# Kernel tuning notes

Hardware: AMD Instinct MI355X
Metric: run time of the kernel (lower is better)

Reference implementation:

```python
import jax, jax.numpy as jnp
import numpy as np

N_NODES = 100000
N_EDGES = 1600000
FEAT = 512
CLS = 64
HID = 200  # each hop layer output width; 3 hops -> 600 concat


def spmm(row, col, vals, x):
    # out[r] = sum_{e: row[e]==r} vals[e] * x[col[e]]  -- sparse A @ x
    return jax.ops.segment_sum(x[col] * vals[:, None], row, num_segments=x.shape[0])


def setup_inputs() -> dict:
    key = jax.random.key(0)
    ks = jax.random.split(key, 12)
    adj_index = jax.random.randint(ks[0], (2, N_EDGES), 0, N_NODES, dtype=jnp.int64)
    # scale like a normalized adjacency (~1/avg_degree) to keep powers stable
    adj_values = jax.random.uniform(ks[1], (N_EDGES,), dtype=jnp.float32) * (1.0 / 16.0)
    features = jax.random.normal(ks[2], (N_NODES, FEAT), dtype=jnp.float32)
    s1 = (2.0 / (FEAT + HID)) ** 0.5
    s2 = (2.0 / (3 * HID + HID)) ** 0.5
    sf = (2.0 / (3 * HID + CLS)) ** 0.5
    W1 = jax.random.normal(ks[3], (3, FEAT, HID), dtype=jnp.float32) * s1
    b1 = jax.random.normal(ks[4], (3, HID), dtype=jnp.float32) * 0.01
    W2 = jax.random.normal(ks[5], (3, 3 * HID, HID), dtype=jnp.float32) * s2
    b2 = jax.random.normal(ks[6], (3, HID), dtype=jnp.float32) * 0.01
    Wfc = jax.random.normal(ks[7], (3 * HID, CLS), dtype=jnp.float32) * sf
    bfc = jax.random.normal(ks[8], (CLS,), dtype=jnp.float32) * 0.01
    return {"adj_index": adj_index, "adj_values": adj_values, "features": features,
            "W1": W1, "b1": b1, "W2": W2, "b2": b2, "Wfc": Wfc, "bfc": bfc}


def reference(adj_index, adj_values, features, W1, b1, W2, b2, Wfc, bfc):
    # Inference mode: dropout is identity.
    row, col = adj_index[0], adj_index[1]
    # upper (sparse) layers: linear + bias + relu, then (iterations-1) spmm hops
    outs1 = []
    for i in range(3):  # iterations = i + 1
        h = jax.nn.relu(features @ W1[i] + b1[i][None, :])
        for _ in range(i):
            h = spmm(row, col, adj_values, h)
        outs1.append(h)
    abstract1 = jnp.concatenate(outs1, axis=1)  # [N, 600]
    # bottom (dense) layers: linear, (iterations-1) spmm hops, then + bias
    outs2 = []
    for i in range(3):
        h = abstract1 @ W2[i]
        for _ in range(i):
            h = spmm(row, col, adj_values, h)
        h = h + b2[i][None, :]
        outs2.append(h)
    abstract2 = jnp.concatenate(outs2, axis=1)  # [N, 600]
    node_emb = abstract2 @ Wfc + bfc  # [N, CLS]
    predictions = jax.nn.log_softmax(node_emb, axis=1)
    return node_emb, predictions
```

## Files before the change

kernel.cpp:

```cpp
#include <hip/hip_runtime.h>

typedef unsigned short u16;
typedef unsigned int u32;
typedef __attribute__((ext_vector_type(8))) short short8;
typedef __attribute__((ext_vector_type(4))) float f32x4;
typedef __attribute__((ext_vector_type(4))) u32 u32x4;
typedef __attribute__((ext_vector_type(2))) u32 u32x2;

#define NN 100000
#define PAD 640

__device__ __forceinline__ float b2f(u16 u) {
    union { u32 i; float f; } v; v.i = ((u32)u) << 16; return v.f;
}
__device__ __forceinline__ u16 f2b(float f) {
    union { float f; u32 i; } v; v.f = f;
    u32 x = v.i;
    return (u16)((x + 0x7FFFu + ((x >> 16) & 1u)) >> 16);
}
__device__ __forceinline__ u32 pack2(float lo, float hi) {
    return (u32)f2b(lo) | ((u32)f2b(hi) << 16);
}
__device__ __forceinline__ float rdf(const void* p, size_t i, int f) {
    return f ? ((const float*)p)[i] : b2f(((const u16*)p)[i]);
}
__device__ __forceinline__ void gload16(const u16* g, u16* l) {
    __builtin_amdgcn_global_load_lds(
        (const __attribute__((address_space(1))) void*)g,
        (__attribute__((address_space(3))) void*)l, 16, 0, 0);
}

__global__ void probe_k(const int* __restrict__ idx,
                        const void* avals, const void* feats, const void* W1,
                        const void* b1, const void* W2, const void* b2,
                        const void* Wfc, const void* bfc,
                        int* __restrict__ flags) {
    if (threadIdx.x != 0 || blockIdx.x != 0) return;
    int z = 1;
    for (int i = 0; i < 128; ++i)
        if (idx[2 * i + 1] != 0) { z = 0; break; }
    flags[0] = z;
    const void* ts[8] = {avals, feats, W1, b1, W2, b2, Wfc, bfc};
    const int ns[8] = {256, 256, 256, 128, 256, 128, 256, 32};
    for (int t = 0; t < 8; ++t) {
        const u16* p = (const u16*)ts[t];
        int n = ns[t], bad = 0;
        for (int i = 0; i < n; ++i) {
            int e = (p[2 * i] >> 7) & 0xFF;
            if (e >= 133) bad++;
        }
        flags[1 + t] = (bad * 8 >= n) ? 1 : 0;
    }
}

__device__ __forceinline__ int load_row(const int* idx, int E, int f, int e) {
    return f ? idx[2 * e] : idx[e];
}
__device__ __forceinline__ int load_col(const int* idx, int E, int f, int e) {
    return f ? idx[2 * E + 2 * e] : idx[E + e];
}

__global__ void featconv_k(const void* __restrict__ src, u16* __restrict__ dst,
                           const int* __restrict__ flags) {
    int i = blockIdx.x * 256 + threadIdx.x;
    if (i >= NN * 512) return;
    int f = flags[2];
    dst[i] = f ? f2b(((const float*)src)[i]) : ((const u16*)src)[i];
}
__global__ void w1t_k(const void* __restrict__ W1, u16* __restrict__ w1t,
                      const int* __restrict__ flags) {
    int i = blockIdx.x * 256 + threadIdx.x;
    if (i >= 640 * 512) return;
    int n = i >> 9, k = i & 511;
    float v = 0.f;
    if (n < 600) {
        int ib = n / 200, c = n % 200;
        v = rdf(W1, (size_t)ib * 102400 + (size_t)k * 200 + c, flags[3]);
    }
    w1t[i] = f2b(v);
}
__global__ void w2t_k(const void* __restrict__ W2, u16* __restrict__ w2t,
                      const int* __restrict__ flags) {
    int i = blockIdx.x * 256 + threadIdx.x;
    if (i >= 640 * 640) return;
    int n = i / 640, k = i % 640;
    float v = 0.f;
    if (n < 600 && k < 600) {
        int ib = n / 200, c = n % 200;
        v = rdf(W2, (size_t)ib * 120000 + (size_t)k * 200 + c, flags[5]);
    }
    w2t[i] = f2b(v);
}
__global__ void wfct_k(const void* __restrict__ Wfc, u16* __restrict__ wfct,
                       const int* __restrict__ flags) {
    int i = blockIdx.x * 256 + threadIdx.x;
    if (i >= 64 * 640) return;
    int n = i / 640, k = i % 640;
    float v = 0.f;
    if (k < 600) v = rdf(Wfc, (size_t)k * 64 + n, flags[7]);
    wfct[i] = f2b(v);
}
__global__ void bconv_k(const void* __restrict__ b1, const void* __restrict__ b2,
                        const void* __restrict__ bfc, float* __restrict__ o,
                        const int* __restrict__ flags) {
    int i = blockIdx.x * 256 + threadIdx.x;
    if (i < 600) o[i] = rdf(b1, i, flags[4]);
    else if (i < 1200) o[i] = rdf(b2, i - 600, flags[6]);
    else if (i < 1264) o[i] = rdf(bfc, i - 1200, flags[8]);
}

__global__ void count_k(const int* __restrict__ idx, int E, const int* __restrict__ flags,
                        int* __restrict__ counts) {
    int e = blockIdx.x * 256 + threadIdx.x;
    if (e >= E) return;
    int r = load_row(idx, E, flags[0], e);
    if ((u32)r >= NN) return;
    atomicAdd(&counts[r], 1);
}

__global__ void chunksum_k(const int* __restrict__ counts, int* __restrict__ chsum) {
    __shared__ int sm[256];
    int c = blockIdx.x, t = threadIdx.x;
    int base = c * 1024, s = 0;
    for (int i = t; i < 1024; i += 256) {
        int g = base + i;
        if (g < NN) s += counts[g];
    }
    sm[t] = s; __syncthreads();
    for (int off = 128; off; off >>= 1) {
        if (t < off) sm[t] += sm[t + off];
        __syncthreads();
    }
    if (t == 0) chsum[c] = sm[0];
}

__global__ void chscan_k(const int* __restrict__ chsum, int nch, int* __restrict__ choff,
                         int* __restrict__ row_ptr, int E) {
    if (threadIdx.x == 0 && blockIdx.x == 0) {
        int run = 0;
        for (int c = 0; c < nch; ++c) { choff[c] = run; run += chsum[c]; }
        row_ptr[NN] = run;
    }
}

__global__ __launch_bounds__(1024) void scan_k(const int* __restrict__ counts,
                                               const int* __restrict__ choff,
                                               int* __restrict__ row_ptr,
                                               int* __restrict__ cursor) {
    __shared__ int sm[1024];
    int c = blockIdx.x, t = threadIdx.x;
    int g = c * 1024 + t;
    int v = (g < NN) ? counts[g] : 0;
    sm[t] = v;
    __syncthreads();
    for (int off = 1; off < 1024; off <<= 1) {
        int add = (t >= off) ? sm[t - off] : 0;
        __syncthreads();
        sm[t] += add;
        __syncthreads();
    }
    if (g < NN) {
        int ex = choff[c] + sm[t] - v;
        row_ptr[g] = ex;
        cursor[g] = ex;
    }
}

__global__ void scatter_k(const int* __restrict__ idx, const void* __restrict__ avals, int E,
                          const int* __restrict__ flags, int* __restrict__ cursor,
                          int* __restrict__ colsS, float* __restrict__ valsS) {
    int e = blockIdx.x * 256 + threadIdx.x;
    if (e >= E) return;
    int f = flags[0];
    int r = load_row(idx, E, f, e);
    if ((u32)r >= NN) return;
    int c = load_col(idx, E, f, e);
    if ((u32)c >= NN) c = 0;
    int p = atomicAdd(&cursor[r], 1);
    colsS[p] = c;
    valsS[p] = rdf(avals, e, flags[1]);
}

__global__ __launch_bounds__(256) void gemm128_k(
    const u16* __restrict__ A, const u16* __restrict__ Bt,
    u16* __restrict__ C, float* __restrict__ Cf,
    const float* __restrict__ bias, int bias_n, int relu,
    int M, int K, int lda, int ldc) {
    __shared__ u16 As[128 * 32];
    __shared__ u16 Bs[128 * 32];
    const int tid = threadIdx.x;
    const int wave = tid >> 6, lane = tid & 63;
    const int bm = blockIdx.x * 128, bn = blockIdx.y * 128;
    const int wrow = (wave >> 1) * 64, wcol = (wave & 1) * 64;
    const int l15 = lane & 15, l4 = lane >> 4;
    f32x4 acc[4][4] = {};

    const int c0 = wave * 2;
    const int rowA0 = c0 * 16 + (lane >> 2);
    const int rowA1 = rowA0 + 16;
    const int colE = (lane & 3) * 8;
    int gr0 = bm + rowA0; if (gr0 >= M) gr0 = M - 1;
    int gr1 = bm + rowA1; if (gr1 >= M) gr1 = M - 1;
    const u16* a0p = A + (size_t)gr0 * lda + colE;
    const u16* a1p = A + (size_t)gr1 * lda + colE;
    const u16* b0p = Bt + (size_t)(bn + rowA0) * K + colE;
    const u16* b1p = Bt + (size_t)(bn + rowA1) * K + colE;
    u16* lA0 = As + c0 * 512;
    u16* lA1 = As + c0 * 512 + 512;
    u16* lB0 = Bs + c0 * 512;
    u16* lB1 = Bs + c0 * 512 + 512;

    for (int k0 = 0; k0 < K; k0 += 32) {
        __syncthreads();
        gload16(a0p + k0, lA0);
        gload16(a1p + k0, lA1);
        gload16(b0p + k0, lB0);
        gload16(b1p + k0, lB1);
        __syncthreads();
        short8 af[4], bf[4];
#pragma unroll
        for (int t = 0; t < 4; ++t) {
            af[t] = *(const short8*)&As[(wrow + t * 16 + l15) * 32 + l4 * 8];
            bf[t] = *(const short8*)&Bs[(wcol + t * 16 + l15) * 32 + l4 * 8];
        }
#pragma unroll
        for (int mi = 0; mi < 4; ++mi)
#pragma unroll
            for (int ni = 0; ni < 4; ++ni)
                acc[mi][ni] = __builtin_amdgcn_mfma_f32_16x16x32_bf16(
                    af[mi], bf[ni], acc[mi][ni], 0, 0, 0);
    }

#pragma unroll
    for (int mi = 0; mi < 4; ++mi)
#pragma unroll
        for (int ni = 0; ni < 4; ++ni)
#pragma unroll
            for (int r4 = 0; r4 < 4; ++r4) {
                int row = bm + wrow + mi * 16 + l4 * 4 + r4;
                int col = bn + wcol + ni * 16 + l15;
                if (row < M) {
                    float v = acc[mi][ni][r4];
                    if (bias && col < bias_n) v += bias[col];
                    if (relu) v = fmaxf(v, 0.0f);
                    if (C) C[(size_t)row * ldc + col] = f2b(v);
                    if (Cf) Cf[(size_t)row * ldc + col] = v;
                }
            }
}

__global__ __launch_bounds__(256) void gemm_k(
    const u16* __restrict__ A, const u16* __restrict__ Bt,
    u16* __restrict__ C, float* __restrict__ Cf,
    const float* __restrict__ bias, int bias_n, int relu,
    int M, int K, int lda, int ldc) {
    __shared__ u16 As[64][40];
    __shared__ u16 Bs[64][40];
    const int tid = threadIdx.x;
    const int wave = tid >> 6, lane = tid & 63;
    const int bm = blockIdx.x * 64, bn = blockIdx.y * 64;
    const int wr = (wave >> 1) * 32, wc = (wave & 1) * 32;
    const int l15 = lane & 15, l4 = lane >> 4;
    f32x4 acc[2][2] = {};

    const int srow = tid >> 2;
    const int skoff = (tid & 3) * 8;
    const bool arow_ok = (bm + srow) < M;
    const u16* aptr = A + (size_t)(bm + srow) * lda + skoff;
    const u16* bptr = Bt + (size_t)(bn + srow) * K + skoff;

    for (int k0 = 0; k0 < K; k0 += 32) {
        short8 av = {};
        if (arow_ok) av = *(const short8*)(aptr + k0);
        short8 bv = *(const short8*)(bptr + k0);
        __syncthreads();
        *(short8*)&As[srow][skoff] = av;
        *(short8*)&Bs[srow][skoff] = bv;
        __syncthreads();
        short8 a0 = *(const short8*)&As[wr + l15][l4 * 8];
        short8 a1 = *(const short8*)&As[wr + 16 + l15][l4 * 8];
        short8 bb0 = *(const short8*)&Bs[wc + l15][l4 * 8];
        short8 bb1 = *(const short8*)&Bs[wc + 16 + l15][l4 * 8];
        acc[0][0] = __builtin_amdgcn_mfma_f32_16x16x32_bf16(a0, bb0, acc[0][0], 0, 0, 0);
        acc[0][1] = __builtin_amdgcn_mfma_f32_16x16x32_bf16(a0, bb1, acc[0][1], 0, 0, 0);
        acc[1][0] = __builtin_amdgcn_mfma_f32_16x16x32_bf16(a1, bb0, acc[1][0], 0, 0, 0);
        acc[1][1] = __builtin_amdgcn_mfma_f32_16x16x32_bf16(a1, bb1, acc[1][1], 0, 0, 0);
    }

#pragma unroll
    for (int mi = 0; mi < 2; ++mi)
#pragma unroll
        for (int ni = 0; ni < 2; ++ni)
#pragma unroll
            for (int r = 0; r < 4; ++r) {
                int row = bm + wr + mi * 16 + l4 * 4 + r;
                int col = bn + wc + ni * 16 + l15;
                if (row < M) {
                    float v = acc[mi][ni][r];
                    if (bias && col < bias_n) v += bias[col];
                    if (relu) v = fmaxf(v, 0.0f);
                    if (C) C[(size_t)row * ldc + col] = f2b(v);
                    if (Cf) Cf[(size_t)row * ldc + col] = v;
                }
            }
}

__global__ __launch_bounds__(256) void spmm400_k(
    const int* __restrict__ row_ptr, const int* __restrict__ cols,
    const float* __restrict__ vals, int E,
    const u16* __restrict__ X, u16* __restrict__ Y1, u16* __restrict__ Yt,
    const float* __restrict__ bias1) {
    int r = blockIdx.x * 4 + (threadIdx.x >> 6);
    if (r >= NN) return;
    int lane = threadIdx.x & 63;
    int s = row_ptr[r], e = row_ptr[r + 1];
    if (e > E) e = E;
    if (s < 0) s = 0;
    if (s > e) s = e;
    float a[8] = {0.f, 0.f, 0.f, 0.f, 0.f, 0.f, 0.f, 0.f};
    const bool act = lane < 50;
    const u32* xb = (const u32*)X;
    int i = s;
    for (; i + 2 <= e; i += 2) {
        int ca = cols[i]; if ((u32)ca >= NN) ca = 0;
        int cb = cols[i + 1]; if ((u32)cb >= NN) cb = 0;
        float va = vals[i], vb = vals[i + 1];
        if (act) {
            u32x4 ga = *(const u32x4*)(xb + (size_t)ca * 320 + lane * 4);
            u32x4 gb = *(const u32x4*)(xb + (size_t)cb * 320 + lane * 4);
#pragma unroll
            for (int q = 0; q < 4; ++q) {
                union { u32 i; float f; } lo, hi;
                lo.i = ga[q] << 16; hi.i = ga[q] & 0xffff0000u;
                a[2 * q] = fmaf(va, lo.f, a[2 * q]);
                a[2 * q + 1] = fmaf(va, hi.f, a[2 * q + 1]);
                lo.i = gb[q] << 16; hi.i = gb[q] & 0xffff0000u;
                a[2 * q] = fmaf(vb, lo.f, a[2 * q]);
                a[2 * q + 1] = fmaf(vb, hi.f, a[2 * q + 1]);
            }
        }
    }
    if (i < e) {
        int ca = cols[i]; if ((u32)ca >= NN) ca = 0;
        float va = vals[i];
        if (act) {
            u32x4 ga = *(const u32x4*)(xb + (size_t)ca * 320 + lane * 4);
#pragma unroll
            for (int q = 0; q < 4; ++q) {
                union { u32 i; float f; } lo, hi;
                lo.i = ga[q] << 16; hi.i = ga[q] & 0xffff0000u;
                a[2 * q] = fmaf(va, lo.f, a[2 * q]);
                a[2 * q + 1] = fmaf(va, hi.f, a[2 * q + 1]);
            }
        }
    }
    if (bias1 && lane < 25) {
#pragma unroll
        for (int q = 0; q < 8; ++q) a[q] += bias1[lane * 8 + q];
    }
    u32x4 o;
    o[0] = pack2(a[0], a[1]); o[1] = pack2(a[2], a[3]);
    o[2] = pack2(a[4], a[5]); o[3] = pack2(a[6], a[7]);
    if (lane < 25) {
        *(u32x4*)((u32*)Y1 + (size_t)r * 320 + lane * 4) = o;
    } else if (lane < 50) {
        *(u32x4*)((u32*)Yt + (size_t)r * 100 + (lane - 25) * 4) = o;
    }
}

__global__ __launch_bounds__(256) void spmm200_k(
    const int* __restrict__ row_ptr, const int* __restrict__ cols,
    const float* __restrict__ vals, int E,
    const u16* __restrict__ X, int ldx,
    u16* __restrict__ Y, int ldy,
    const float* __restrict__ bias) {
    int r = blockIdx.x * 4 + (threadIdx.x >> 6);
    if (r >= NN) return;
    int lane = threadIdx.x & 63;
    int s = row_ptr[r], e = row_ptr[r + 1];
    if (e > E) e = E;
    if (s < 0) s = 0;
    if (s > e) s = e;
    float a[4] = {0.f, 0.f, 0.f, 0.f};
    const bool act = lane < 50;
    const int ldxw = ldx >> 1, ldyw = ldy >> 1;
    const u32* xb = (const u32*)X;
    int i = s;
    for (; i + 2 <= e; i += 2) {
        int ca = cols[i]; if ((u32)ca >= NN) ca = 0;
        int cb = cols[i + 1]; if ((u32)cb >= NN) cb = 0;
        float va = vals[i], vb = vals[i + 1];
        if (act) {
            u32x2 ga = *(const u32x2*)(xb + (size_t)ca * ldxw + lane * 2);
            u32x2 gb = *(const u32x2*)(xb + (size_t)cb * ldxw + lane * 2);
#pragma unroll
            for (int q = 0; q < 2; ++q) {
                union { u32 i; float f; } lo, hi;
                lo.i = ga[q] << 16; hi.i = ga[q] & 0xffff0000u;
                a[2 * q] = fmaf(va, lo.f, a[2 * q]);
                a[2 * q + 1] = fmaf(va, hi.f, a[2 * q + 1]);
                lo.i = gb[q] << 16; hi.i = gb[q] & 0xffff0000u;
                a[2 * q] = fmaf(vb, lo.f, a[2 * q]);
                a[2 * q + 1] = fmaf(vb, hi.f, a[2 * q + 1]);
            }
        }
    }
    if (i < e) {
        int ca = cols[i]; if ((u32)ca >= NN) ca = 0;
        float va = vals[i];
        if (act) {
            u32x2 ga = *(const u32x2*)(xb + (size_t)ca * ldxw + lane * 2);
#pragma unroll
            for (int q = 0; q < 2; ++q) {
                union { u32 i; float f; } lo, hi;
                lo.i = ga[q] << 16; hi.i = ga[q] & 0xffff0000u;
                a[2 * q] = fmaf(va, lo.f, a[2 * q]);
                a[2 * q + 1] = fmaf(va, hi.f, a[2 * q + 1]);
            }
        }
    }
    if (bias && act) {
#pragma unroll
        for (int q = 0; q < 4; ++q) a[q] += bias[lane * 4 + q];
    }
    if (act) {
        u32x2 o;
        o[0] = pack2(a[0], a[1]); o[1] = pack2(a[2], a[3]);
        *(u32x2*)((u32*)Y + (size_t)r * ldyw + lane * 2) = o;
    }
}

__global__ void copyblk_k(const u16* __restrict__ src, u16* __restrict__ dst) {
    int i = blockIdx.x * 256 + threadIdx.x;
    if (i >= NN * 100) return;
    int r = i / 100, c = i % 100;
    ((u32*)dst)[(size_t)r * 320 + c] = ((const u32*)src)[(size_t)r * 320 + c];
}
__global__ void zeropad_k(u16* __restrict__ dst) {
    int i = blockIdx.x * 256 + threadIdx.x;
    if (i >= NN * 20) return;
    int r = i / 20, c = i % 20;
    ((u32*)dst)[(size_t)r * 320 + 300 + c] = 0u;
}
__global__ void copybias_k(const u16* __restrict__ src, u16* __restrict__ dst,
                           const float* __restrict__ bias) {
    int i = blockIdx.x * 256 + threadIdx.x;
    if (i >= NN * 200) return;
    int r = i / 200, c = i % 200;
    dst[(size_t)r * 640 + c] = f2b(b2f(src[(size_t)r * 640 + c]) + bias[c]);
}

__global__ void softmax_k(const float* __restrict__ ne, float* __restrict__ out) {
    int r = blockIdx.x * 4 + (threadIdx.x >> 6);
    if (r >= NN) return;
    int lane = threadIdx.x & 63;
    float v = ne[(size_t)r * 64 + lane];
    float m = v;
    for (int off = 32; off; off >>= 1) m = fmaxf(m, __shfl_xor(m, off, 64));
    float e = expf(v - m);
    float ssum = e;
    for (int off = 32; off; off >>= 1) ssum += __shfl_xor(ssum, off, 64);
    out[(size_t)r * 64 + lane] = v - m - logf(ssum);
}

extern "C" void kernel_launch(void* const* d_in, const int* in_sizes, int n_in,
                              void* d_out, int out_size, void* d_ws, size_t ws_size,
                              hipStream_t stream) {
    const int* adj_idx = (const int*)d_in[0];
    const void* adj_vals = d_in[1];
    const void* feats = d_in[2];
    const void* W1 = d_in[3];
    const void* b1 = d_in[4];
    const void* W2 = d_in[5];
    const void* b2 = d_in[6];
    const void* Wfc = d_in[7];
    const void* bfc = d_in[8];
    const int E = in_sizes[1];
    (void)n_in; (void)out_size; (void)ws_size;

    char* ws = (char*)d_ws;
    size_t off = 0;
    auto alloc = [&](size_t b) { size_t o = off; off += (b + 255) & ~(size_t)255; return o; };
    u16* buf0 = (u16*)(ws + alloc((size_t)NN * PAD * 2));
    u16* buf1 = (u16*)(ws + alloc((size_t)NN * PAD * 2));
    u16* hop = (u16*)(ws + alloc((size_t)NN * 200 * 2));
    u16* w1t = (u16*)(ws + alloc((size_t)640 * 512 * 2));
    u16* w2t = (u16*)(ws + alloc((size_t)640 * 640 * 2));
    u16* wfct = (u16*)(ws + alloc((size_t)64 * 640 * 2));
    float* biasf = (float*)(ws + alloc(1264 * 4));
    int* counts = (int*)(ws + alloc((size_t)NN * 4));
    int* cursor = (int*)(ws + alloc((size_t)NN * 4));
    int* row_ptr = (int*)(ws + alloc((size_t)(NN + 1) * 4));
    int* chsum = (int*)(ws + alloc(4096));
    int* choff = (int*)(ws + alloc(4096));
    int* flags = (int*)(ws + alloc(256));
    int* colsS = (int*)(ws + alloc((size_t)E * 4));
    float* valsS = (float*)(ws + alloc((size_t)E * 4));

    u16* featsB = buf1;
    float* out_ne = (float*)d_out;
    float* out_pred = out_ne + (size_t)NN * 64;

    probe_k<<<1, 64, 0, stream>>>(adj_idx, adj_vals, feats, W1, b1, W2, b2, Wfc, bfc, flags);
    featconv_k<<<(NN * 512 + 255) / 256, 256, 0, stream>>>(feats, featsB, flags);
    w1t_k<<<(640 * 512 + 255) / 256, 256, 0, stream>>>(W1, w1t, flags);
    w2t_k<<<(640 * 640 + 255) / 256, 256, 0, stream>>>(W2, w2t, flags);
    wfct_k<<<(64 * 640 + 255) / 256, 256, 0, stream>>>(Wfc, wfct, flags);
    bconv_k<<<5, 256, 0, stream>>>(b1, b2, bfc, biasf, flags);

    hipMemsetAsync(counts, 0, NN * 4, stream);
    count_k<<<(E + 255) / 256, 256, 0, stream>>>(adj_idx, E, flags, counts);
    const int NCH = (NN + 1023) / 1024;
    chunksum_k<<<NCH, 256, 0, stream>>>(counts, chsum);
    chscan_k<<<1, 64, 0, stream>>>(chsum, NCH, choff, row_ptr, E);
    scan_k<<<NCH, 1024, 0, stream>>>(counts, choff, row_ptr, cursor);
    scatter_k<<<(E + 255) / 256, 256, 0, stream>>>(adj_idx, adj_vals, E, flags, cursor, colsS, valsS);

    dim3 g128((NN + 127) / 128, PAD / 128);
    gemm128_k<<<g128, 256, 0, stream>>>(featsB, w1t, buf0, nullptr, biasf, 600, 1, NN, 512, 512, PAD);
    copyblk_k<<<(NN * 100 + 255) / 256, 256, 0, stream>>>(buf0, buf1);
    zeropad_k<<<(NN * 20 + 255) / 256, 256, 0, stream>>>(buf1);
    spmm400_k<<<(NN + 3) / 4, 256, 0, stream>>>(row_ptr, colsS, valsS, E,
                                                buf0 + 200, buf1 + 200, hop, nullptr);
    spmm200_k<<<(NN + 3) / 4, 256, 0, stream>>>(row_ptr, colsS, valsS, E,
                                                hop, 200, buf1 + 400, PAD, nullptr);
    gemm128_k<<<g128, 256, 0, stream>>>(buf1, w2t, buf0, nullptr, nullptr, 0, 0, NN, PAD, PAD, PAD);
    copybias_k<<<(NN * 200 + 255) / 256, 256, 0, stream>>>(buf0, buf1, biasf + 600);
    spmm400_k<<<(NN + 3) / 4, 256, 0, stream>>>(row_ptr, colsS, valsS, E,
                                                buf0 + 200, buf1 + 200, hop, biasf + 800);
    spmm200_k<<<(NN + 3) / 4, 256, 0, stream>>>(row_ptr, colsS, valsS, E,
                                                hop, 200, buf1 + 400, PAD, biasf + 1000);
    dim3 gC((NN + 63) / 64, 1);
    gemm_k<<<gC, 256, 0, stream>>>(buf1, wfct, nullptr, out_ne, biasf + 1200, 64, 0, NN, PAD, PAD, 64);
    softmax_k<<<(NN + 3) / 4, 256, 0, stream>>>(out_ne, out_pred);
}
```

Before: 1.727 ms.

## Interleave CSR col/val pairs, unroll SpMM by four, merge prep kernels, swap GEMM grid

Stores each sorted edge's column and value together as one 8-byte pair, so the SpMM kernels fetch both with a single load instead of two separate arrays. The SpMM inner loops are unrolled from two to four edges to put more independent gathers in flight. The three weight-transpose kernels and the bias conversion are merged into one launch. The GEMM grid is transposed so blocks sharing an A row-tile run next to each other, which may improve L2 reuse of A.

```diff
diff --git a/kernel.cpp b/kernel.cpp
--- a/kernel.cpp
+++ b/kernel.cpp
@@ -21,6 +21,9 @@
 __device__ __forceinline__ u32 pack2(float lo, float hi) {
     return (u32)f2b(lo) | ((u32)f2b(hi) << 16);
 }
+__device__ __forceinline__ float u2f(u32 u) {
+    union { u32 i; float f; } v; v.i = u; return v.f;
+}
 __device__ __forceinline__ float rdf(const void* p, size_t i, int f) {
     return f ? ((const float*)p)[i] : b2f(((const u16*)p)[i]);
 }
@@ -28,6 +31,20 @@
     __builtin_amdgcn_global_load_lds(
         (const __attribute__((address_space(1))) void*)g,
         (__attribute__((address_space(3))) void*)l, 16, 0, 0);
+}
+__device__ __forceinline__ void acc8(float* a, u32x4 g, float v) {
+#pragma unroll
+    for (int q = 0; q < 4; ++q) {
+        a[2 * q] = fmaf(v, u2f(g[q] << 16), a[2 * q]);
+        a[2 * q + 1] = fmaf(v, u2f(g[q] & 0xffff0000u), a[2 * q + 1]);
+    }
+}
+__device__ __forceinline__ void acc4(float* a, u32x2 g, float v) {
+#pragma unroll
+    for (int q = 0; q < 2; ++q) {
+        a[2 * q] = fmaf(v, u2f(g[q] << 16), a[2 * q]);
+        a[2 * q + 1] = fmaf(v, u2f(g[q] & 0xffff0000u), a[2 * q + 1]);
+    }
 }
 
 __global__ void probe_k(const int* __restrict__ idx,
@@ -67,46 +84,43 @@
     int f = flags[2];
     dst[i] = f ? f2b(((const float*)src)[i]) : ((const u16*)src)[i];
 }
-__global__ void w1t_k(const void* __restrict__ W1, u16* __restrict__ w1t,
-                      const int* __restrict__ flags) {
-    int i = blockIdx.x * 256 + threadIdx.x;
-    if (i >= 640 * 512) return;
-    int n = i >> 9, k = i & 511;
-    float v = 0.f;
-    if (n < 600) {
-        int ib = n / 200, c = n % 200;
-        v = rdf(W1, (size_t)ib * 102400 + (size_t)k * 200 + c, flags[3]);
-    }
-    w1t[i] = f2b(v);
-}
-__global__ void w2t_k(const void* __restrict__ W2, u16* __restrict__ w2t,
-                      const int* __restrict__ flags) {
-    int i = blockIdx.x * 256 + threadIdx.x;
-    if (i >= 640 * 640) return;
-    int n = i / 640, k = i % 640;
-    float v = 0.f;
-    if (n < 600 && k < 600) {
-        int ib = n / 200, c = n % 200;
-        v = rdf(W2, (size_t)ib * 120000 + (size_t)k * 200 + c, flags[5]);
-    }
-    w2t[i] = f2b(v);
-}
-__global__ void wfct_k(const void* __restrict__ Wfc, u16* __restrict__ wfct,
+__global__ void prep_k(const void* __restrict__ W1, const void* __restrict__ W2,
+                       const void* __restrict__ Wfc,
+                       const void* __restrict__ b1, const void* __restrict__ b2,
+                       const void* __restrict__ bfc,
+                       u16* __restrict__ w1t, u16* __restrict__ w2t,
+                       u16* __restrict__ wfct, float* __restrict__ biasf,
                        const int* __restrict__ flags) {
     int i = blockIdx.x * 256 + threadIdx.x;
-    if (i >= 64 * 640) return;
-    int n = i / 640, k = i % 640;
-    float v = 0.f;
-    if (k < 600) v = rdf(Wfc, (size_t)k * 64 + n, flags[7]);
-    wfct[i] = f2b(v);
-}
-__global__ void bconv_k(const void* __restrict__ b1, const void* __restrict__ b2,
-                        const void* __restrict__ bfc, float* __restrict__ o,
-                        const int* __restrict__ flags) {
-    int i = blockIdx.x * 256 + threadIdx.x;
-    if (i < 600) o[i] = rdf(b1, i, flags[4]);
-    else if (i < 1200) o[i] = rdf(b2, i - 600, flags[6]);
-    else if (i < 1264) o[i] = rdf(bfc, i - 1200, flags[8]);
+    if (i < 327680) {
+        int n = i >> 9, k = i & 511;
+        float v = 0.f;
+        if (n < 600) {
+            int ib = n / 200, c = n % 200;
+            v = rdf(W1, (size_t)ib * 102400 + (size_t)k * 200 + c, flags[3]);
+        }
+        w1t[i] = f2b(v);
+    } else if (i < 737280) {
+        int j = i - 327680;
+        int n = j / 640, k = j % 640;
+        float v = 0.f;
+        if (n < 600 && k < 600) {
+            int ib = n / 200, c = n % 200;
+            v = rdf(W2, (size_t)ib * 120000 + (size_t)k * 200 + c, flags[5]);
+        }
+        w2t[j] = f2b(v);
+    } else if (i < 778240) {
+        int j = i - 737280;
+        int n = j / 640, k = j % 640;
+        float v = 0.f;
+        if (k < 600) v = rdf(Wfc, (size_t)k * 64 + n, flags[7]);
+        wfct[j] = f2b(v);
+    } else if (i < 779504) {
+        int j = i - 778240;
+        if (j < 600) biasf[j] = rdf(b1, j, flags[4]);
+        else if (j < 1200) biasf[j] = rdf(b2, j - 600, flags[6]);
+        else biasf[j] = rdf(bfc, j - 1200, flags[8]);
+    }
 }
 
 __global__ void count_k(const int* __restrict__ idx, int E, const int* __restrict__ flags,
@@ -168,7 +182,7 @@
 
 __global__ void scatter_k(const int* __restrict__ idx, const void* __restrict__ avals, int E,
                           const int* __restrict__ flags, int* __restrict__ cursor,
-                          int* __restrict__ colsS, float* __restrict__ valsS) {
+                          u32x2* __restrict__ cvS) {
     int e = blockIdx.x * 256 + threadIdx.x;
     if (e >= E) return;
     int f = flags[0];
@@ -177,8 +191,10 @@
     int c = load_col(idx, E, f, e);
     if ((u32)c >= NN) c = 0;
     int p = atomicAdd(&cursor[r], 1);
-    colsS[p] = c;
-    valsS[p] = rdf(avals, e, flags[1]);
+    float v = rdf(avals, e, flags[1]);
+    union { float f; u32 i; } vb; vb.f = v;
+    u32x2 o; o[0] = (u32)c; o[1] = vb.i;
+    cvS[p] = o;
 }
 
 __global__ __launch_bounds__(256) void gemm128_k(
@@ -190,7 +206,7 @@
     __shared__ u16 Bs[128 * 32];
     const int tid = threadIdx.x;
     const int wave = tid >> 6, lane = tid & 63;
-    const int bm = blockIdx.x * 128, bn = blockIdx.y * 128;
+    const int bm = blockIdx.y * 128, bn = blockIdx.x * 128;
     const int wrow = (wave >> 1) * 64, wcol = (wave & 1) * 64;
     const int l15 = lane & 15, l4 = lane >> 4;
     f32x4 acc[4][4] = {};
@@ -306,8 +322,7 @@
 }
 
 __global__ __launch_bounds__(256) void spmm400_k(
-    const int* __restrict__ row_ptr, const int* __restrict__ cols,
-    const float* __restrict__ vals, int E,
+    const int* __restrict__ row_ptr, const u32x2* __restrict__ cv, int E,
     const u16* __restrict__ X, u16* __restrict__ Y1, u16* __restrict__ Yt,
     const float* __restrict__ bias1) {
     int r = blockIdx.x * 4 + (threadIdx.x >> 6);
@@ -320,38 +335,31 @@
     float a[8] = {0.f, 0.f, 0.f, 0.f, 0.f, 0.f, 0.f, 0.f};
     const bool act = lane < 50;
     const u32* xb = (const u32*)X;
+    const size_t lo = (size_t)lane * 4;
     int i = s;
-    for (; i + 2 <= e; i += 2) {
-        int ca = cols[i]; if ((u32)ca >= NN) ca = 0;
-        int cb = cols[i + 1]; if ((u32)cb >= NN) cb = 0;
-        float va = vals[i], vb = vals[i + 1];
+    for (; i + 4 <= e; i += 4) {
+        u32x2 p0 = cv[i], p1 = cv[i + 1], p2 = cv[i + 2], p3 = cv[i + 3];
+        int c0 = p0[0]; if ((u32)c0 >= NN) c0 = 0;
+        int c1 = p1[0]; if ((u32)c1 >= NN) c1 = 0;
+        int c2 = p2[0]; if ((u32)c2 >= NN) c2 = 0;
+        int c3 = p3[0]; if ((u32)c3 >= NN) c3 = 0;
         if (act) {
-            u32x4 ga = *(const u32x4*)(xb + (size_t)ca * 320 + lane * 4);
-            u32x4 gb = *(const u32x4*)(xb + (size_t)cb * 320 + lane * 4);
-#pragma unroll
-            for (int q = 0; q < 4; ++q) {
-                union { u32 i; float f; } lo, hi;
-                lo.i = ga[q] << 16; hi.i = ga[q] & 0xffff0000u;
-                a[2 * q] = fmaf(va, lo.f, a[2 * q]);
-                a[2 * q + 1] = fmaf(va, hi.f, a[2 * q + 1]);
-                lo.i = gb[q] << 16; hi.i = gb[q] & 0xffff0000u;
-                a[2 * q] = fmaf(vb, lo.f, a[2 * q]);
-                a[2 * q + 1] = fmaf(vb, hi.f, a[2 * q + 1]);
-            }
-        }
-    }
-    if (i < e) {
-        int ca = cols[i]; if ((u32)ca >= NN) ca = 0;
-        float va = vals[i];
+            u32x4 g0 = *(const u32x4*)(xb + (size_t)c0 * 320 + lo);
+            u32x4 g1 = *(const u32x4*)(xb + (size_t)c1 * 320 + lo);
+            u32x4 g2 = *(const u32x4*)(xb + (size_t)c2 * 320 + lo);
+            u32x4 g3 = *(const u32x4*)(xb + (size_t)c3 * 320 + lo);
+            acc8(a, g0, u2f(p0[1]));
+            acc8(a, g1, u2f(p1[1]));
+            acc8(a, g2, u2f(p2[1]));
+            acc8(a, g3, u2f(p3[1]));
+        }
+    }
+    for (; i < e; ++i) {
+        u32x2 p = cv[i];
+        int c = p[0]; if ((u32)c >= NN) c = 0;
         if (act) {
-            u32x4 ga = *(const u32x4*)(xb + (size_t)ca * 320 + lane * 4);
-#pragma unroll
-            for (int q = 0; q < 4; ++q) {
-                union { u32 i; float f; } lo, hi;
-                lo.i = ga[q] << 16; hi.i = ga[q] & 0xffff0000u;
-                a[2 * q] = fmaf(va, lo.f, a[2 * q]);
-                a[2 * q + 1] = fmaf(va, hi.f, a[2 * q + 1]);
-            }
+            u32x4 g = *(const u32x4*)(xb + (size_t)c * 320 + lo);
+            acc8(a, g, u2f(p[1]));
         }
     }
     if (bias1 && lane < 25) {
@@ -369,8 +377,7 @@
 }
 
 __global__ __launch_bounds__(256) void spmm200_k(
-    const int* __restrict__ row_ptr, const int* __restrict__ cols,
-    const float* __restrict__ vals, int E,
+    const int* __restrict__ row_ptr, const u32x2* __restrict__ cv, int E,
     const u16* __restrict__ X, int ldx,
     u16* __restrict__ Y, int ldy,
     const float* __restrict__ bias) {
@@ -385,38 +392,31 @@
     const bool act = lane < 50;
     const int ldxw = ldx >> 1, ldyw = ldy >> 1;
     const u32* xb = (const u32*)X;
+    const size_t lo = (size_t)lane * 2;
     int i = s;
-    for (; i + 2 <= e; i += 2) {
-        int ca = cols[i]; if ((u32)ca >= NN) ca = 0;
-        int cb = cols[i + 1]; if ((u32)cb >= NN) cb = 0;
-        float va = vals[i], vb = vals[i + 1];
+    for (; i + 4 <= e; i += 4) {
+        u32x2 p0 = cv[i], p1 = cv[i + 1], p2 = cv[i + 2], p3 = cv[i + 3];
+        int c0 = p0[0]; if ((u32)c0 >= NN) c0 = 0;
+        int c1 = p1[0]; if ((u32)c1 >= NN) c1 = 0;
+        int c2 = p2[0]; if ((u32)c2 >= NN) c2 = 0;
+        int c3 = p3[0]; if ((u32)c3 >= NN) c3 = 0;
         if (act) {
-            u32x2 ga = *(const u32x2*)(xb + (size_t)ca * ldxw + lane * 2);
-            u32x2 gb = *(const u32x2*)(xb + (size_t)cb * ldxw + lane * 2);
-#pragma unroll
-            for (int q = 0; q < 2; ++q) {
-                union { u32 i; float f; } lo, hi;
-                lo.i = ga[q] << 16; hi.i = ga[q] & 0xffff0000u;
-                a[2 * q] = fmaf(va, lo.f, a[2 * q]);
-                a[2 * q + 1] = fmaf(va, hi.f, a[2 * q + 1]);
-                lo.i = gb[q] << 16; hi.i = gb[q] & 0xffff0000u;
-                a[2 * q] = fmaf(vb, lo.f, a[2 * q]);
-                a[2 * q + 1] = fmaf(vb, hi.f, a[2 * q + 1]);
-            }
-        }
-    }
-    if (i < e) {
-        int ca = cols[i]; if ((u32)ca >= NN) ca = 0;
-        float va = vals[i];
+            u32x2 g0 = *(const u32x2*)(xb + (size_t)c0 * ldxw + lo);
+            u32x2 g1 = *(const u32x2*)(xb + (size_t)c1 * ldxw + lo);
+            u32x2 g2 = *(const u32x2*)(xb + (size_t)c2 * ldxw + lo);
+            u32x2 g3 = *(const u32x2*)(xb + (size_t)c3 * ldxw + lo);
+            acc4(a, g0, u2f(p0[1]));
+            acc4(a, g1, u2f(p1[1]));
+            acc4(a, g2, u2f(p2[1]));
+            acc4(a, g3, u2f(p3[1]));
+        }
+    }
+    for (; i < e; ++i) {
+        u32x2 p = cv[i];
+        int c = p[0]; if ((u32)c >= NN) c = 0;
         if (act) {
-            u32x2 ga = *(const u32x2*)(xb + (size_t)ca * ldxw + lane * 2);
-#pragma unroll
-            for (int q = 0; q < 2; ++q) {
-                union { u32 i; float f; } lo, hi;
-                lo.i = ga[q] << 16; hi.i = ga[q] & 0xffff0000u;
-                a[2 * q] = fmaf(va, lo.f, a[2 * q]);
-                a[2 * q + 1] = fmaf(va, hi.f, a[2 * q + 1]);
-            }
+            u32x2 g = *(const u32x2*)(xb + (size_t)c * ldxw + lo);
+            acc4(a, g, u2f(p[1]));
         }
     }
     if (bias && act) {
@@ -426,7 +426,7 @@
     if (act) {
         u32x2 o;
         o[0] = pack2(a[0], a[1]); o[1] = pack2(a[2], a[3]);
-        *(u32x2*)((u32*)Y + (size_t)r * ldyw + lane * 2) = o;
+        *(u32x2*)((u32*)Y + (size_t)r * ldyw + lo) = o;
     }
 }
 
@@ -494,8 +494,7 @@
     int* chsum = (int*)(ws + alloc(4096));
     int* choff = (int*)(ws + alloc(4096));
     int* flags = (int*)(ws + alloc(256));
-    int* colsS = (int*)(ws + alloc((size_t)E * 4));
-    float* valsS = (float*)(ws + alloc((size_t)E * 4));
+    u32x2* cvS = (u32x2*)(ws + alloc((size_t)E * 8));
 
     u16* featsB = buf1;
     float* out_ne = (float*)d_out;
@@ -503,10 +502,8 @@
 
     probe_k<<<1, 64, 0, stream>>>(adj_idx, adj_vals, feats, W1, b1, W2, b2, Wfc, bfc, flags);
     featconv_k<<<(NN * 512 + 255) / 256, 256, 0, stream>>>(feats, featsB, flags);
-    w1t_k<<<(640 * 512 + 255) / 256, 256, 0, stream>>>(W1, w1t, flags);
-    w2t_k<<<(640 * 640 + 255) / 256, 256, 0, stream>>>(W2, w2t, flags);
-    wfct_k<<<(64 * 640 + 255) / 256, 256, 0, stream>>>(Wfc, wfct, flags);
-    bconv_k<<<5, 256, 0, stream>>>(b1, b2, bfc, biasf, flags);
+    prep_k<<<(779504 + 255) / 256, 256, 0, stream>>>(W1, W2, Wfc, b1, b2, bfc,
+                                                     w1t, w2t, wfct, biasf, flags);
 
     hipMemsetAsync(counts, 0, NN * 4, stream);
     count_k<<<(E + 255) / 256, 256, 0, stream>>>(adj_idx, E, flags, counts);
@@ -514,22 +511,18 @@
     chunksum_k<<<NCH, 256, 0, stream>>>(counts, chsum);
     chscan_k<<<1, 64, 0, stream>>>(chsum, NCH, choff, row_ptr, E);
     scan_k<<<NCH, 1024, 0, stream>>>(counts, choff, row_ptr, cursor);
-    scatter_k<<<(E + 255) / 256, 256, 0, stream>>>(adj_idx, adj_vals, E, flags, cursor, colsS, valsS);
-
-    dim3 g128((NN + 127) / 128, PAD / 128);
+    scatter_k<<<(E + 255) / 256, 256, 0, stream>>>(adj_idx, adj_vals, E, flags, cursor, cvS);
+
+    dim3 g128(PAD / 128, (NN + 127) / 128);
     gemm128_k<<<g128, 256, 0, stream>>>(featsB, w1t, buf0, nullptr, biasf, 600, 1, NN, 512, 512, PAD);
     copyblk_k<<<(NN * 100 + 255) / 256, 256, 0, stream>>>(buf0, buf1);
     zeropad_k<<<(NN * 20 + 255) / 256, 256, 0, stream>>>(buf1);
-    spmm400_k<<<(NN + 3) / 4, 256, 0, stream>>>(row_ptr, colsS, valsS, E,
-                                                buf0 + 200, buf1 + 200, hop, nullptr);
-    spmm200_k<<<(NN + 3) / 4, 256, 0, stream>>>(row_ptr, colsS, valsS, E,
-                                                hop, 200, buf1 + 400, PAD, nullptr);
+    spmm400_k<<<(NN + 3) / 4, 256, 0, stream>>>(row_ptr, cvS, E, buf0 + 200, buf1 + 200, hop, nullptr);
+    spmm200_k<<<(NN + 3) / 4, 256, 0, stream>>>(row_ptr, cvS, E, hop, 200, buf1 + 400, PAD, nullptr);
     gemm128_k<<<g128, 256, 0, stream>>>(buf1, w2t, buf0, nullptr, nullptr, 0, 0, NN, PAD, PAD, PAD);
     copybias_k<<<(NN * 200 + 255) / 256, 256, 0, stream>>>(buf0, buf1, biasf + 600);
-    spmm400_k<<<(NN + 3) / 4, 256, 0, stream>>>(row_ptr, colsS, valsS, E,
-                                                buf0 + 200, buf1 + 200, hop, biasf + 800);
-    spmm200_k<<<(NN + 3) / 4, 256, 0, stream>>>(row_ptr, colsS, valsS, E,
-                                                hop, 200, buf1 + 400, PAD, biasf + 1000);
+    spmm400_k<<<(NN + 3) / 4, 256, 0, stream>>>(row_ptr, cvS, E, buf0 + 200, buf1 + 200, hop, biasf + 800);
+    spmm200_k<<<(NN + 3) / 4, 256, 0, stream>>>(row_ptr, cvS, E, hop, 200, buf1 + 400, PAD, biasf + 1000);
     dim3 gC((NN + 63) / 64, 1);
     gemm_k<<<gC, 256, 0, stream>>>(buf1, wfct, nullptr, out_ne, biasf + 1200, 64, 0, NN, PAD, PAD, 64);
     softmax_k<<<(NN + 3) / 4, 256, 0, stream>>>(out_ne, out_pred);
```

New measurement: 1.735 ms. No clear change (+0.5%).
